# Optimization experiments

Hardware: AMD Instinct MI355X
Metric: run time of the kernel (lower is better)

Reference implementation:

```python
import jax, jax.numpy as jnp
import numpy as np

B, L, H, V, HALF = 128, 4096, 64, 64, 32
ALPHA = 0.95
LN_EPS = 1e-5


def _normalize(x):
    # torch F.normalize(dim=-1): x / max(||x||_2, 1e-12)
    n = jnp.linalg.norm(x, axis=-1, keepdims=True)
    return x / jnp.maximum(n, 1e-12)


def setup_inputs() -> dict:
    key = jax.random.key(0)
    ks = jax.random.split(key, 17)
    s = 0.05
    return {
        "seq": jax.random.randint(ks[0], (B, L), 0, V),
        "embed": jax.random.normal(ks[1], (V, H), jnp.float32),
        "W1": jax.random.normal(ks[2], (H, 2 * H), jnp.float32) * s,
        "b1": jnp.zeros((2 * H,), jnp.float32),
        "W2": jax.random.normal(ks[3], (2 * H, H), jnp.float32) * s,
        "b2": jnp.zeros((H,), jnp.float32),
        "gamma": jnp.ones((H,), jnp.float32),
        "beta": jnp.zeros((H,), jnp.float32),
        "Ws": jax.random.normal(ks[4], (H, HALF), jnp.float32) * s,
        "bs": jnp.zeros((HALF,), jnp.float32),
        "We": jax.random.normal(ks[5], (H, HALF), jnp.float32) * s,
        "be": jnp.zeros((HALF,), jnp.float32),
        "Wrp": jax.random.normal(ks[6], (2 * HALF, H), jnp.float32) * s,
        "brp": jnp.zeros((H,), jnp.float32),
        "Wout": jax.random.normal(ks[7], (H, V), jnp.float32) * s,
        "bout": jnp.zeros((V,), jnp.float32),
    }


def _forward(seq, embed, W1, b1, W2, b2, gamma, beta,
             Ws, bs, We, be, Wrp, brp, Wout, bout):
    # Encoder: embed + FF(ReLU) residual + LayerNorm
    h0 = embed[seq]                                   # [B,L,H]
    ff = jnp.maximum(h0 @ W1 + b1, 0.0) @ W2 + b2
    x = h0 + ff
    mu = x.mean(-1, keepdims=True)
    var = ((x - mu) ** 2).mean(-1, keepdims=True)
    h = (x - mu) / jnp.sqrt(var + LN_EPS) * gamma + beta  # [B,L,H]

    # Precompute per-step projections for t = 0 .. L-2
    hp = h[:, :-1, :]                                 # [B,L-1,H]
    hs = hp @ Ws + bs                                 # [B,L-1,HALF]
    he = hp @ We + be
    ksn = _normalize(hs)
    ken = _normalize(he)
    scale = (jnp.arange(L - 1, dtype=h.dtype) + 1.0) / L  # (t+1)/L

    def step(carry, inp):
        M_s, M_e = carry                              # [B,HALF,HALF]
        hs_t, he_t, ks_t, ke_t, sc = inp
        vps = jnp.einsum('bij,bj->bi', M_s, ks_t)
        vpe = jnp.einsum('bij,bj->bi', M_e, ke_t)
        M_s = M_s + (1.0 - ALPHA) * (hs_t - vps)[:, :, None] * ks_t[:, None, :]
        M_e = M_e + (1.0 - ALPHA) * sc * (he_t - vpe)[:, :, None] * ke_t[:, None, :]
        return (M_s, M_e), None

    xs = (jnp.swapaxes(hs, 0, 1), jnp.swapaxes(he, 0, 1),
          jnp.swapaxes(ksn, 0, 1), jnp.swapaxes(ken, 0, 1), scale)
    M0 = jnp.zeros((B, HALF, HALF), h.dtype)
    (M_s, M_e), _ = jax.lax.scan(step, (M0, M0), xs)

    # Read with last-token query
    q = h[:, -1, :]
    qs = _normalize(q @ Ws + bs)
    qe = _normalize(q @ We + be)
    rs = jnp.einsum('bij,bj->bi', M_s, qs)
    re = jnp.einsum('bij,bj->bi', M_e, qe)
    r = jnp.concatenate([rs, re], axis=-1)            # [B,2*HALF]
    return (r @ Wrp + brp) @ Wout + bout              # [B,V]


def reference(seq, embed, W1, b1, W2, b2, gamma, beta,
              Ws, bs, We, be, Wrp, brp, Wout, bout):
    return _forward(seq, embed, W1, b1, W2, b2, gamma, beta,
                    Ws, bs, We, be, Wrp, brp, Wout, bout)
```

## Files before the change

### kernel.cpp

```cpp
#include <hip/hip_runtime.h>
#include <hip/hip_bf16.h>
#include <stdint.h>


#define BETA 0.05f
#define NB 128
#define NL 4096
#define TC 16
#define NCH 256
#define NBLD 6
#define SLOT_F 336
#define NSLOT 12

#define L_GR   (NSLOT * SLOT_F)
#define L_DA   (L_GR + 4096)
#define L_RV   (L_DA + 64)
#define L_O1   (L_RV + 64)
#define L_WHO  (L_O1 + 64)
#define L_TOT  (L_WHO + 1)

struct Ptrs { const void* p[15]; };

__device__ inline float readlane_f(float v, int l) {
    return __int_as_float(__builtin_amdgcn_readlane(__float_as_int(v), l));
}
__device__ inline float ldT(const float* p, int i) { return p[i]; }
__device__ inline float ldT(const __hip_bfloat16* p, int i) { return __bfloat162float(p[i]); }

template <typename T>
__device__ void build_tables_body(const T* emb, const T* W1, const T* b1,
                                  const T* W2, const T* b2, const T* gam,
                                  const T* bet, const T* Wsm, const T* bsv,
                                  const T* Wem, const T* bev, float* tbl)
{
    int v = blockIdx.x;
    int j = threadIdx.x;
    __shared__ float h0s[64];
    __shared__ float act[128];
    __shared__ float hrow[64];

    float h0 = ldT(emb, v * 64 + j);
    h0s[j] = h0;
    __syncthreads();

    float za = ldT(b1, j);
    float zb = ldT(b1, j + 64);
    for (int k = 0; k < 64; ++k) {
        float hk = h0s[k];
        za = fmaf(hk, ldT(W1, k * 128 + j), za);
        zb = fmaf(hk, ldT(W1, k * 128 + j + 64), zb);
    }
    act[j] = fmaxf(za, 0.0f);
    act[j + 64] = fmaxf(zb, 0.0f);
    __syncthreads();

    float ff = ldT(b2, j);
    for (int k = 0; k < 128; ++k)
        ff = fmaf(act[k], ldT(W2, k * 64 + j), ff);
    float x = h0 + ff;

    float s = x;
    for (int off = 32; off >= 1; off >>= 1) s += __shfl_xor(s, off, 64);
    float mu = s * (1.0f / 64.0f);
    float d = x - mu;
    float s2 = d * d;
    for (int off = 32; off >= 1; off >>= 1) s2 += __shfl_xor(s2, off, 64);
    float var = s2 * (1.0f / 64.0f);
    float h = d / sqrtf(var + 1e-5f) * ldT(gam, j) + ldT(bet, j);
    hrow[j] = h;
    __syncthreads();

    if (j < 32) {
        float sv = ldT(bsv, j);
        for (int k = 0; k < 64; ++k)
            sv = fmaf(hrow[k], ldT(Wsm, k * 32 + j), sv);
        float n2 = sv * sv;
        for (int off = 16; off >= 1; off >>= 1) n2 += __shfl_xor(n2, off, 64);
        float nrm = fmaxf(sqrtf(n2), 1e-12f);
        tbl[v * 32 + j] = sv;
        tbl[2048 + v * 32 + j] = sv / nrm;
    } else {
        int jj = j - 32;
        float ev = ldT(bev, jj);
        for (int k = 0; k < 64; ++k)
            ev = fmaf(hrow[k], ldT(Wem, k * 32 + jj), ev);
        float n2 = ev * ev;
        for (int off = 16; off >= 1; off >>= 1) n2 += __shfl_xor(n2, off, 64);
        float nrm = fmaxf(sqrtf(n2), 1e-12f);
        tbl[4096 + v * 32 + jj] = ev;
        tbl[6144 + v * 32 + jj] = ev / nrm;
    }
}

__global__ __launch_bounds__(64, 2) void build_tables(Ptrs ps, float* __restrict__ tbl,
                                                      int* __restrict__ flags)
{
    if (blockIdx.x == 0) {
        flags[threadIdx.x] = 0;
        flags[threadIdx.x + 64] = 0;
    }
    uint32_t g0 = *(const uint32_t*)ps.p[5];
    if (g0 == 0x3F803F80u)
        build_tables_body((const __hip_bfloat16*)ps.p[0], (const __hip_bfloat16*)ps.p[1],
                          (const __hip_bfloat16*)ps.p[2], (const __hip_bfloat16*)ps.p[3],
                          (const __hip_bfloat16*)ps.p[4], (const __hip_bfloat16*)ps.p[5],
                          (const __hip_bfloat16*)ps.p[6], (const __hip_bfloat16*)ps.p[7],
                          (const __hip_bfloat16*)ps.p[8], (const __hip_bfloat16*)ps.p[9],
                          (const __hip_bfloat16*)ps.p[10], tbl);
    else
        build_tables_body((const float*)ps.p[0], (const float*)ps.p[1],
                          (const float*)ps.p[2], (const float*)ps.p[3],
                          (const float*)ps.p[4], (const float*)ps.p[5],
                          (const float*)ps.p[6], (const float*)ps.p[7],
                          (const float*)ps.p[8], (const float*)ps.p[9],
                          (const float*)ps.p[10], tbl);
}

__global__ __launch_bounds__(512, 1) void ema_ms(
    const int* __restrict__ seq, const float* __restrict__ tbl,
    Ptrs ps, float* __restrict__ rvbuf, int* __restrict__ flags,
    void* __restrict__ outv)
{
    __shared__ __align__(16) float S[L_TOT];

    int bm = blockIdx.x;
    int b = bm >> 1, mat = bm & 1;
    int tid = threadIdx.x;
    int wid = tid >> 6, lane = tid & 63;
    const float bstep = BETA / 4096.0f;

    if (tid < 64) S[L_DA + tid] = 0.0f;

    const float* ktab = tbl + 2048 + mat * 4096;
    for (int i = tid; i < 2048; i += 512)
        S[(i >> 5) * 33 + (i & 31)] = ktab[i];
    __syncthreads();

    {
        float Kown[32];
#pragma unroll
        for (int j = 0; j < 32; ++j) Kown[j] = S[lane * 33 + j];
        for (int v8 = 0; v8 < 8; ++v8) {
            int vt = wid * 8 + v8;
            float acc = 0.0f;
#pragma unroll
            for (int j = 0; j < 32; ++j)
                acc = fmaf(S[vt * 33 + j], Kown[j], acc);
            S[L_GR + vt * 64 + lane] = acc;
        }
    }
    __syncthreads();

    const int* sb = seq + (size_t)b * NL;
    float y = 0.0f;
    if (wid == 0) {
        int vlast = sb[NL - 1];
        y = S[L_GR + vlast * 64 + lane];
    }

    const int NRND = (NCH + NBLD - 1) / NBLD;

    for (int r = 0; r <= NRND; ++r) {
        if (wid != 0 && wid != 4) {
            int bi = (wid > 4) ? (wid - 2) : (wid - 1);
            int ci = NBLD * r + bi;
            if (r < NRND && ci < NCH) {
                int c = NCH - 1 - ci;
                float* slot = S + ((r & 1) * NBLD + bi) * SLOT_F;
                int tokv = 0; float bneg = 0.0f;
                if (lane < TC) {
                    int t = c * TC + (TC - 1) - lane;
                    tokv = sb[t];
                    float bb = mat ? bstep * (float)(t + 1) : BETA;
                    if (t == NL - 1) bb = 0.0f;
                    bneg = -bb;
                    ((int*)(slot + 320))[lane] = tokv;
                }
                float garr[TC];
#pragma unroll
                for (int p = 0; p < TC; ++p) {
                    int vp = __builtin_amdgcn_readlane(tokv, p);
                    garr[p] = S[L_GR + vp * 64 + tokv] * bneg;
                }
                float z[TC];
                z[15] = (lane == 15) ? 1.0f : 0.0f;
#pragma unroll
                for (int q = TC - 2; q >= 0; --q) {
                    float zq = (lane == q) ? 1.0f : 0.0f;
#pragma unroll
                    for (int j = q + 1; j < TC; ++j)
                        zq = fmaf(readlane_f(garr[j], q), z[j], zq);
                    z[q] = zq;
                }
                if (lane < TC) {
                    float4* vd = (float4*)(slot + lane * 20);
                    vd[0] = make_float4(z[0], z[1], z[2], z[3]);
                    vd[1] = make_float4(z[4], z[5], z[6], z[7]);
                    vd[2] = make_float4(z[8], z[9], z[10], z[11]);
                    vd[3] = make_float4(z[12], z[13], z[14], z[15]);
                }
            }
        } else if (wid == 0 && r >= 1) {
            int rpar = ((r - 1) & 1) * NBLD;
            int base_ci = NBLD * (r - 1);
            int nch_r = NCH - base_ci;
            if (nch_r > NBLD) nch_r = NBLD;

            float* slot0 = S + rpar * SLOT_F;
            int tokc = ((int*)(slot0 + 320))[lane & 15];
            int stokc[16];
#pragma unroll
            for (int q = 0; q < 16; ++q)
                stokc[q] = __builtin_amdgcn_readlane(tokc, q);
            const float4* vr0 = (const float4*)(slot0 + (lane & 15) * 20);
            float4 Vc0 = vr0[0], Vc1 = vr0[1], Vc2 = vr0[2], Vc3 = vr0[3];
            float gpc[16];
#pragma unroll
            for (int p = 0; p < 16; ++p)
                gpc[p] = S[L_GR + stokc[p] * 64 + lane];

            for (int bi = 0; bi < nch_r; ++bi) {
                int c = NCH - 1 - (base_ci + bi);

                int bin = (bi + 1 < nch_r) ? (bi + 1) : bi;
                float* slotn = S + (rpar + bin) * SLOT_F;
                int tokn = ((int*)(slotn + 320))[lane & 15];
                int stokn[16];
#pragma unroll
                for (int q = 0; q < 16; ++q)
                    stokn[q] = __builtin_amdgcn_readlane(tokn, q);
                const float4* vrn = (const float4*)(slotn + (lane & 15) * 20);
                float4 Vn0 = vrn[0], Vn1 = vrn[1], Vn2 = vrn[2], Vn3 = vrn[3];
                float gpn[16];
#pragma unroll
                for (int p = 0; p < 16; ++p)
                    gpn[p] = S[L_GR + stokn[p] * 64 + lane];
                asm volatile("" ::: "memory");

                float bv = 0.0f;
                if (lane < TC) {
                    int t = c * TC + (TC - 1) - lane;
                    float bb = mat ? bstep * (float)(t + 1) : BETA;
                    if (t == NL - 1) bb = 0.0f;
                    bv = bb;
                }
                float ryq[16];
#pragma unroll
                for (int q = 0; q < 16; ++q)
                    ryq[q] = readlane_f(y, stokc[q]);
                float s0 = Vc0.x * ryq[0];
                float s1 = Vc0.y * ryq[1];
                float s2 = Vc0.z * ryq[2];
                float s3 = Vc0.w * ryq[3];
                s0 = fmaf(Vc1.x, ryq[4], s0);
                s1 = fmaf(Vc1.y, ryq[5], s1);
                s2 = fmaf(Vc1.z, ryq[6], s2);
                s3 = fmaf(Vc1.w, ryq[7], s3);
                s0 = fmaf(Vc2.x, ryq[8], s0);
                s1 = fmaf(Vc2.y, ryq[9], s1);
                s2 = fmaf(Vc2.z, ryq[10], s2);
                s3 = fmaf(Vc2.w, ryq[11], s3);
                s0 = fmaf(Vc3.x, ryq[12], s0);
                s1 = fmaf(Vc3.y, ryq[13], s1);
                s2 = fmaf(Vc3.z, ryq[14], s2);
                s3 = fmaf(Vc3.w, ryq[15], s3);
                float dv = ((s0 + s1) + (s2 + s3)) * bv;
                float dn = -dv;
                float ya = 0.f, yb = 0.f, yc2 = 0.f, yd = 0.f;
#pragma unroll
                for (int p = 0; p < TC; p += 4) {
                    ya  = fmaf(readlane_f(dn, p),     gpc[p],     ya);
                    yb  = fmaf(readlane_f(dn, p + 1), gpc[p + 1], yb);
                    yc2 = fmaf(readlane_f(dn, p + 2), gpc[p + 2], yc2);
                    yd  = fmaf(readlane_f(dn, p + 3), gpc[p + 3], yd);
                }
                y += (ya + yb) + (yc2 + yd);
                if (lane < TC) atomicAdd(&S[L_DA + tokc], dv);

                tokc = tokn;
#pragma unroll
                for (int q = 0; q < 16; ++q) stokc[q] = stokn[q];
                Vc0 = Vn0; Vc1 = Vn1; Vc2 = Vn2; Vc3 = Vn3;
#pragma unroll
                for (int p = 0; p < 16; ++p) gpc[p] = gpn[p];
            }
        }
        __syncthreads();
    }

    if (tid < 32) {
        float rr = 0.0f;
        const float* hsrc = tbl + mat * 4096;
        for (int v = 0; v < 64; ++v)
            rr = fmaf(S[L_DA + v], hsrc[v * 32 + tid], rr);
        __hip_atomic_store(&rvbuf[bm * 32 + tid], rr,
                           __ATOMIC_RELAXED, __HIP_MEMORY_SCOPE_AGENT);
    }
    __syncthreads();
    if (tid == 0) {
        int old = __hip_atomic_fetch_add(&flags[b], 1,
                                         __ATOMIC_ACQ_REL, __HIP_MEMORY_SCOPE_AGENT);
        ((int*)S)[L_WHO] = old;
    }
    __syncthreads();
    if (((int*)S)[L_WHO] != 1) return;

    if (tid < 64)
        S[L_RV + tid] = __hip_atomic_load(&rvbuf[b * 64 + tid],
                                          __ATOMIC_RELAXED, __HIP_MEMORY_SCOPE_AGENT);
    __syncthreads();

    uint32_t g0h = *(const uint32_t*)ps.p[5];
    int isbf = (g0h == 0x3F803F80u) ? 1 : 0;
    if (tid < 64) {
        float o;
        if (isbf) {
            const __hip_bfloat16* W = (const __hip_bfloat16*)ps.p[11];
            o = __bfloat162float(((const __hip_bfloat16*)ps.p[12])[tid]);
            for (int i = 0; i < 64; ++i)
                o = fmaf(S[L_RV + i], __bfloat162float(W[i * 64 + tid]), o);
        } else {
            const float* W = (const float*)ps.p[11];
            o = ((const float*)ps.p[12])[tid];
            for (int i = 0; i < 64; ++i)
                o = fmaf(S[L_RV + i], W[i * 64 + tid], o);
        }
        S[L_O1 + tid] = o;
    }
    __syncthreads();
    if (tid < 64) {
        float o2;
        if (isbf) {
            const __hip_bfloat16* W = (const __hip_bfloat16*)ps.p[13];
            o2 = __bfloat162float(((const __hip_bfloat16*)ps.p[14])[tid]);
            for (int i = 0; i < 64; ++i)
                o2 = fmaf(S[L_O1 + i], __bfloat162float(W[i * 64 + tid]), o2);
            ((__hip_bfloat16*)outv)[b * 64 + tid] = __float2bfloat16(o2);
        } else {
            const float* W = (const float*)ps.p[13];
            o2 = ((const float*)ps.p[14])[tid];
            for (int i = 0; i < 64; ++i)
                o2 = fmaf(S[L_O1 + i], W[i * 64 + tid], o2);
            ((float*)outv)[b * 64 + tid] = o2;
        }
    }
}

extern "C" void kernel_launch(void* const* d_in, const int* in_sizes, int n_in,
                              void* d_out, int out_size, void* d_ws, size_t ws_size,
                              hipStream_t stream) {
    const int* seq = (const int*)d_in[0];
    Ptrs ps;
    for (int i = 0; i < 15; ++i) ps.p[i] = d_in[i + 1];

    float* tbl = (float*)d_ws;
    float* rvbuf = tbl + 8192;
    int* flags = (int*)(rvbuf + 8192);

    build_tables<<<64, 64, 0, stream>>>(ps, tbl, flags);
    ema_ms<<<NB * 2, 512, 0, stream>>>(seq, tbl, ps, rvbuf, flags, d_out);
}
```

Measured before the change: 200.8 us.

## Batch chunk building into 32-chunk segments to cut block barriers

Builder warps now fill a double-buffered segment of 32 chunks per round instead of 6, and the consumer warp walks the whole segment. This reduces the number of __syncthreads rounds from about 43 to 9, which lowers barrier and idle overhead on the serial consumer path. In exchange, LDS use for slot buffers grows substantially, and the load across builder warps is uneven because 32 chunks do not split evenly over 6 builders.

```diff
diff --git a/kernel.cpp b/kernel.cpp
--- a/kernel.cpp
+++ b/kernel.cpp
@@ -10,9 +10,11 @@
 #define NCH 256
 #define NBLD 6
 #define SLOT_F 336
-#define NSLOT 12
-
-#define L_GR   (NSLOT * SLOT_F)
+#define SEG_CH 32
+#define SEG_F (SEG_CH * SLOT_F)
+#define NSEG 8
+
+#define L_GR   (2 * SEG_F)
 #define L_DA   (L_GR + 4096)
 #define L_RV   (L_DA + 64)
 #define L_O1   (L_RV + 64)
@@ -128,6 +130,7 @@
     int tid = threadIdx.x;
     int wid = tid >> 6, lane = tid & 63;
     const float bstep = BETA / 4096.0f;
+    const int* sb = seq + (size_t)b * NL;
 
     if (tid < 64) S[L_DA + tid] = 0.0f;
 
@@ -151,22 +154,23 @@
     }
     __syncthreads();
 
-    const int* sb = seq + (size_t)b * NL;
     float y = 0.0f;
     if (wid == 0) {
         int vlast = sb[NL - 1];
         y = S[L_GR + vlast * 64 + lane];
     }
 
-    const int NRND = (NCH + NBLD - 1) / NBLD;
-
-    for (int r = 0; r <= NRND; ++r) {
-        if (wid != 0 && wid != 4) {
-            int bi = (wid > 4) ? (wid - 2) : (wid - 1);
-            int ci = NBLD * r + bi;
-            if (r < NRND && ci < NCH) {
+    int isbld = (wid != 0 && wid != 4);
+    int bi = (wid > 4) ? (wid - 2) : (wid - 1);
+
+    for (int s = -1; s < NSEG; ++s) {
+        if (isbld && s < NSEG - 1) {
+            int sg = s + 1;
+            float* buf = S + (sg & 1) * SEG_F;
+            for (int j = bi; j < SEG_CH; j += NBLD) {
+                int ci = sg * SEG_CH + j;
                 int c = NCH - 1 - ci;
-                float* slot = S + ((r & 1) * NBLD + bi) * SLOT_F;
+                float* slot = buf + j * SLOT_F;
                 int tokv = 0; float bneg = 0.0f;
                 if (lane < TC) {
                     int t = c * TC + (TC - 1) - lane;
@@ -188,8 +192,8 @@
                 for (int q = TC - 2; q >= 0; --q) {
                     float zq = (lane == q) ? 1.0f : 0.0f;
 #pragma unroll
-                    for (int j = q + 1; j < TC; ++j)
-                        zq = fmaf(readlane_f(garr[j], q), z[j], zq);
+                    for (int j2 = q + 1; j2 < TC; ++j2)
+                        zq = fmaf(readlane_f(garr[j2], q), z[j2], zq);
                     z[q] = zq;
                 }
                 if (lane < TC) {
@@ -200,30 +204,27 @@
                     vd[3] = make_float4(z[12], z[13], z[14], z[15]);
                 }
             }
-        } else if (wid == 0 && r >= 1) {
-            int rpar = ((r - 1) & 1) * NBLD;
-            int base_ci = NBLD * (r - 1);
-            int nch_r = NCH - base_ci;
-            if (nch_r > NBLD) nch_r = NBLD;
-
-            float* slot0 = S + rpar * SLOT_F;
-            int tokc = ((int*)(slot0 + 320))[lane & 15];
+        } else if (wid == 0 && s >= 0) {
+            float* buf = S + (s & 1) * SEG_F;
+            int ci0 = s * SEG_CH;
+
+            int tokc = ((int*)(buf + 320))[lane & 15];
             int stokc[16];
 #pragma unroll
             for (int q = 0; q < 16; ++q)
                 stokc[q] = __builtin_amdgcn_readlane(tokc, q);
-            const float4* vr0 = (const float4*)(slot0 + (lane & 15) * 20);
+            const float4* vr0 = (const float4*)(buf + (lane & 15) * 20);
             float4 Vc0 = vr0[0], Vc1 = vr0[1], Vc2 = vr0[2], Vc3 = vr0[3];
             float gpc[16];
 #pragma unroll
             for (int p = 0; p < 16; ++p)
                 gpc[p] = S[L_GR + stokc[p] * 64 + lane];
 
-            for (int bi = 0; bi < nch_r; ++bi) {
-                int c = NCH - 1 - (base_ci + bi);
-
-                int bin = (bi + 1 < nch_r) ? (bi + 1) : bi;
-                float* slotn = S + (rpar + bin) * SLOT_F;
+            for (int j = 0; j < SEG_CH; ++j) {
+                int c = NCH - 1 - (ci0 + j);
+
+                int jn = (j + 1 < SEG_CH) ? (j + 1) : j;
+                float* slotn = buf + jn * SLOT_F;
                 int tokn = ((int*)(slotn + 320))[lane & 15];
                 int stokn[16];
 #pragma unroll
```

Result: slower. 218.9 us (+9.0%).
